# Optimization experiments

Measured on AMD Instinct MI355X. Metric: run time of the kernel, lower is better.

The kernel has to match this reference:

```python
import jax, jax.numpy as jnp
import numpy as np

N_CONTEXT = 256  # teacher-forced prefix length (n_context)
N_INPUTS = 2
HID = 16         # LSTM hidden_size
PROJ = 2         # LSTM proj_size


def setup_inputs() -> dict:
    key = jax.random.key(0)
    ks = jax.random.split(key, 6)
    B, T = 4096, 1024
    s = 1.0 / np.sqrt(HID)  # torch LSTM init range
    return {
        "u_train": jax.random.normal(ks[0], (B, T, N_INPUTS + PROJ), jnp.float32),
        "w_ih": jax.random.uniform(ks[1], (4 * HID, N_INPUTS), jnp.float32, -s, s),
        "w_hh": jax.random.uniform(ks[2], (4 * HID, PROJ), jnp.float32, -s, s),
        "b_ih": jax.random.uniform(ks[3], (4 * HID,), jnp.float32, -s, s),
        "b_hh": jax.random.uniform(ks[4], (4 * HID,), jnp.float32, -s, s),
        "w_hr": jax.random.uniform(ks[5], (PROJ, HID), jnp.float32, -s, s),
    }


def _cell(x, h, c, w_ih, w_hh, b, w_hr):
    # PyTorch LSTM gate order: i, f, g, o; projected output h = (o*tanh(c)) @ w_hr.T
    gates = x @ w_ih.T + h @ w_hh.T + b  # [B, 4*HID]
    i, f, g, o = jnp.split(gates, 4, axis=-1)
    c_new = jax.nn.sigmoid(f) * c + jax.nn.sigmoid(i) * jnp.tanh(g)
    h_new = (jax.nn.sigmoid(o) * jnp.tanh(c_new)) @ w_hr.T  # [B, PROJ]
    return h_new, c_new


def reference(u_train, w_ih, w_hh, b_ih, b_hh, w_hr):
    B = u_train.shape[0]
    u = u_train[..., :N_INPUTS]   # [B, T, 2] exogenous inputs
    y = u_train[..., N_INPUTS:]
    b = b_ih + b_hh

    xs_est = (jnp.swapaxes(u[:, :N_CONTEXT], 0, 1),  # [nstep, B, 2]
              jnp.swapaxes(y[:, :N_CONTEXT], 0, 1))
    c0 = jnp.zeros((B, HID), u_train.dtype)

    def est_step(c, xy):
        x_t, y_t = xy
        h_new, c_new = _cell(x_t, y_t, c, w_ih, w_hh, b, w_hr)
        return c_new, h_new

    cn, h_est = jax.lax.scan(est_step, c0, xs_est)  # h_est: [nstep, B, 2]
    hn = h_est[-1]

    # ---- predict_state: free-running LSTM from (hn, cn) ----
    def pred_step(carry, x_t):
        h, c = carry
        h_new, c_new = _cell(x_t, h, c, w_ih, w_hh, b, w_hr)
        return (h_new, c_new), h_new

    _, h_pred = jax.lax.scan(pred_step, (hn, cn), jnp.swapaxes(u[:, N_CONTEXT:], 0, 1))

    return jnp.concatenate([jnp.swapaxes(h_est, 0, 1), jnp.swapaxes(h_pred, 0, 1)], axis=1)
```

## Files before the change

kernel.cpp:

```cpp
#include <hip/hip_runtime.h>

#define N_CTX  256
#define T_LEN  1024
#define N_SEQ  4096
#define CHUNK  16

__device__ __forceinline__ float fexp2(float x){ return __builtin_amdgcn_exp2f(x); }
__device__ __forceinline__ float frcp (float x){ return __builtin_amdgcn_rcpf(x); }

__device__ __forceinline__ float sigm(float x){
    return frcp(1.0f + fexp2(-1.4426950408889634f * x));
}
__device__ __forceinline__ float tanh_fast(float x){
    float a = fexp2(fminf(2.8853901631790583f * x, 126.0f));
    return (a - 1.0f) * frcp(a + 1.0f);
}

template<int CTRL>
__device__ __forceinline__ float dpp_add(float x){
    int y = __builtin_amdgcn_mov_dpp(__float_as_int(x), CTRL, 0xf, 0xf, true);
    return x + __int_as_float(y);
}
__device__ __forceinline__ float red16(float x){
    x = dpp_add<0xB1>(x);
    x = dpp_add<0x4E>(x);
    x = dpp_add<0x124>(x);
    x = dpp_add<0x128>(x);
    return x;
}

struct LaneW {
    float wi0[4], wi1[4], wh0[4], wh1[4], bs[4];
    float whr0, whr1;
};

template<bool TEACHER>
__device__ __forceinline__ void lstm_step(const float4 x, const LaneW& L,
                                          float& c, float& rh0, float& rh1)
{
    const float h0 = TEACHER ? x.z : rh0;
    const float h1 = TEACHER ? x.w : rh1;
    float g[4];
#pragma unroll
    for (int q = 0; q < 4; ++q)
        g[q] = fmaf(h1, L.wh1[q], fmaf(h0, L.wh0[q],
               fmaf(x.y, L.wi1[q], fmaf(x.x, L.wi0[q], L.bs[q]))));
    const float si = sigm(g[0]);
    const float sf = sigm(g[1]);
    const float tg = tanh_fast(g[2]);
    const float so = sigm(g[3]);
    c = fmaf(sf, c, si * tg);
    const float s = so * tanh_fast(c);
    rh0 = red16(s * L.whr0);
    rh1 = red16(s * L.whr1);
}

__device__ __forceinline__ void load_chunk(float4* b, const float4* __restrict__ up, int base){
#pragma unroll
    for (int i = 0; i < CHUNK; ++i) b[i] = up[base + i];
}

template<bool TEACHER>
__device__ __forceinline__ void compute_chunk(const float4* b, int base, const LaneW& L,
                                              float& c, float& rh0, float& rh1,
                                              float2* __restrict__ op, int j)
{
#pragma unroll
    for (int i = 0; i < CHUNK; ++i) {
        lstm_step<TEACHER>(b[i], L, c, rh0, rh1);
        if (j == 0) op[base + i] = make_float2(rh0, rh1);
    }
}

__global__ __launch_bounds__(256) void openlstm_kernel(
    const float* __restrict__ u,
    const float* __restrict__ w_ih,
    const float* __restrict__ w_hh,
    const float* __restrict__ b_ih,
    const float* __restrict__ b_hh,
    const float* __restrict__ w_hr,
    float* __restrict__ out)
{
    const int tid = blockIdx.x * blockDim.x + threadIdx.x;
    const int seq = tid >> 4;
    const int j   = tid & 15;

    LaneW L;
#pragma unroll
    for (int q = 0; q < 4; ++q) {
        const int row = q * 16 + j;
        L.wi0[q] = w_ih[row*2+0];
        L.wi1[q] = w_ih[row*2+1];
        L.wh0[q] = w_hh[row*2+0];
        L.wh1[q] = w_hh[row*2+1];
        L.bs[q]  = b_ih[row] + b_hh[row];
    }
    L.whr0 = w_hr[j];
    L.whr1 = w_hr[16+j];

    const float4* __restrict__ up = (const float4*)u + (size_t)seq * T_LEN;
    float2* __restrict__ op = (float2*)out + (size_t)seq * T_LEN;

    float c = 0.0f, rh0 = 0.0f, rh1 = 0.0f;
    float4 bufA[CHUNK], bufB[CHUNK];

    load_chunk(bufA, up, 0);

#pragma unroll 1
    for (int base = 0; base < N_CTX; base += 2*CHUNK) {
        load_chunk(bufB, up, base + CHUNK);
        compute_chunk<true>(bufA, base, L, c, rh0, rh1, op, j);
        load_chunk(bufA, up, base + 2*CHUNK);
        compute_chunk<true>(bufB, base + CHUNK, L, c, rh0, rh1, op, j);
    }

#pragma unroll 1
    for (int base = N_CTX; base < T_LEN; base += 2*CHUNK) {
        load_chunk(bufB, up, base + CHUNK);
        compute_chunk<false>(bufA, base, L, c, rh0, rh1, op, j);
        if (base + 2*CHUNK < T_LEN)
            load_chunk(bufA, up, base + 2*CHUNK);
        compute_chunk<false>(bufB, base + CHUNK, L, c, rh0, rh1, op, j);
    }
}

extern "C" void kernel_launch(void* const* d_in, const int* in_sizes, int n_in,
                              void* d_out, int out_size, void* d_ws, size_t ws_size,
                              hipStream_t stream) {
    const float* u    = (const float*)d_in[0];
    const float* w_ih = (const float*)d_in[1];
    const float* w_hh = (const float*)d_in[2];
    const float* b_ih = (const float*)d_in[3];
    const float* b_hh = (const float*)d_in[4];
    const float* w_hr = (const float*)d_in[5];
    float* out = (float*)d_out;

    const int threads = 256;
    const int blocks  = (N_SEQ * 16) / threads;
    hipLaunchKernelGGL(openlstm_kernel, dim3(blocks), dim3(threads), 0, stream,
                       u, w_ih, w_hh, b_ih, b_hh, w_hr, out);
}
```

Baseline: 256.4 us.

## Precompute input gate terms per chunk, fuse sigmoid-tanh divisions, pack FMAs, vectorize stores

Moves the input-dependent gate contributions (x·W_ih + bias) off the serial recurrence by computing them for a whole chunk ahead of the chain, using packed 2-wide FMAs. Inside each step it merges sigmoid(i)*tanh(g) and sigmoid(o)*tanh(c) into single reciprocals, so each step issues fewer rcp instructions on the dependent path. Outputs are now buffered and written as float4 pairs every four steps instead of one float2 per step, the two loops are merged into one chunk loop with a prefetch distance of two chunks, and launch bounds request one block per CU. The per-chunk transformed arrays and deeper prefetch raise register pressure.

```diff
diff --git a/kernel.cpp b/kernel.cpp
--- a/kernel.cpp
+++ b/kernel.cpp
@@ -4,17 +4,18 @@
 #define T_LEN  1024
 #define N_SEQ  4096
 #define CHUNK  16
+#define NCHUNK (T_LEN / CHUNK)
+#define CTXCK  (N_CTX / CHUNK)
+
+typedef float v2f __attribute__((ext_vector_type(2)));
 
 __device__ __forceinline__ float fexp2(float x){ return __builtin_amdgcn_exp2f(x); }
 __device__ __forceinline__ float frcp (float x){ return __builtin_amdgcn_rcpf(x); }
+__device__ __forceinline__ v2f pk_fma(v2f a, v2f b, v2f c){ return __builtin_elementwise_fma(a, b, c); }
 
-__device__ __forceinline__ float sigm(float x){
-    return frcp(1.0f + fexp2(-1.4426950408889634f * x));
-}
-__device__ __forceinline__ float tanh_fast(float x){
-    float a = fexp2(fminf(2.8853901631790583f * x, 126.0f));
-    return (a - 1.0f) * frcp(a + 1.0f);
-}
+#define L1C 1.4426950408889634f
+#define L2C 2.8853901631790583f
+#define ECLAMP 60.0f
 
 template<int CTRL>
 __device__ __forceinline__ float dpp_add(float x){
@@ -30,49 +31,78 @@
 }
 
 struct LaneW {
-    float wi0[4], wi1[4], wh0[4], wh1[4], bs[4];
+    v2f wi0_if, wi1_if, wi0_go, wi1_go;
+    v2f wh0_if, wh1_if, wh0_go, wh1_go;
+    v2f bs_if, bs_go;
     float whr0, whr1;
 };
 
-template<bool TEACHER>
-__device__ __forceinline__ void lstm_step(const float4 x, const LaneW& L,
-                                          float& c, float& rh0, float& rh1)
-{
-    const float h0 = TEACHER ? x.z : rh0;
-    const float h1 = TEACHER ? x.w : rh1;
-    float g[4];
-#pragma unroll
-    for (int q = 0; q < 4; ++q)
-        g[q] = fmaf(h1, L.wh1[q], fmaf(h0, L.wh0[q],
-               fmaf(x.y, L.wi1[q], fmaf(x.x, L.wi0[q], L.bs[q]))));
-    const float si = sigm(g[0]);
-    const float sf = sigm(g[1]);
-    const float tg = tanh_fast(g[2]);
-    const float so = sigm(g[3]);
-    c = fmaf(sf, c, si * tg);
-    const float s = so * tanh_fast(c);
-    rh0 = red16(s * L.whr0);
-    rh1 = red16(s * L.whr1);
-}
+struct ChunkX {
+    v2f   xif[CHUNK];
+    v2f   xgo[CHUNK];
+    float y0[CHUNK];
+    float y1[CHUNK];
+};
 
 __device__ __forceinline__ void load_chunk(float4* b, const float4* __restrict__ up, int base){
 #pragma unroll
     for (int i = 0; i < CHUNK; ++i) b[i] = up[base + i];
 }
 
-template<bool TEACHER>
-__device__ __forceinline__ void compute_chunk(const float4* b, int base, const LaneW& L,
-                                              float& c, float& rh0, float& rh1,
-                                              float2* __restrict__ op, int j)
-{
+__device__ __forceinline__ void transform_chunk(ChunkX& X, const float4* raw, const LaneW& L){
 #pragma unroll
     for (int i = 0; i < CHUNK; ++i) {
-        lstm_step<TEACHER>(b[i], L, c, rh0, rh1);
-        if (j == 0) op[base + i] = make_float2(rh0, rh1);
+        const float4 x = raw[i];
+        v2f xx = {x.x, x.x}, xy = {x.y, x.y};
+        X.xif[i] = pk_fma(xy, L.wi1_if, pk_fma(xx, L.wi0_if, L.bs_if));
+        X.xgo[i] = pk_fma(xy, L.wi1_go, pk_fma(xx, L.wi0_go, L.bs_go));
+        X.y0[i]  = x.z;
+        X.y1[i]  = x.w;
     }
 }
 
-__global__ __launch_bounds__(256) void openlstm_kernel(
+template<bool TEACHER>
+__device__ __forceinline__ void lstm_step(v2f xif, v2f xgo, float y0, float y1,
+                                          const LaneW& L, float& c, float& rh0, float& rh1)
+{
+    const float h0 = TEACHER ? y0 : rh0;
+    const float h1 = TEACHER ? y1 : rh1;
+    v2f hh0 = {h0, h0}, hh1 = {h1, h1};
+    v2f gif = pk_fma(hh1, L.wh1_if, pk_fma(hh0, L.wh0_if, xif));
+    v2f ggo = pk_fma(hh1, L.wh1_go, pk_fma(hh0, L.wh0_go, xgo));
+    const float u  = fexp2(fminf(gif.x * -L1C, ECLAMP));
+    const float ef = fexp2(fminf(gif.y * -L1C, ECLAMP));
+    const float v  = fexp2(fminf(ggo.x *  L2C, ECLAMP));
+    const float eo = fexp2(fminf(ggo.y * -L1C, ECLAMP));
+    const float sf   = frcp(1.0f + ef);
+    const float sitg = (v - 1.0f) * frcp((1.0f + u) * (v + 1.0f));
+    c = fmaf(sf, c, sitg);
+    const float w = fexp2(fminf(c * L2C, ECLAMP));
+    const float s = (w - 1.0f) * frcp((1.0f + eo) * (w + 1.0f));
+    rh0 = red16(s * L.whr0);
+    rh1 = red16(s * L.whr1);
+}
+
+template<bool TEACHER>
+__device__ __forceinline__ void chain_chunk(const ChunkX& X, int baseT, const LaneW& L,
+                                            float& c, float& rh0, float& rh1,
+                                            float4* __restrict__ opv, bool store_lane)
+{
+    float o[8];
+#pragma unroll
+    for (int i = 0; i < CHUNK; ++i) {
+        lstm_step<TEACHER>(X.xif[i], X.xgo[i], X.y0[i], X.y1[i], L, c, rh0, rh1);
+        o[(i & 3) * 2]     = rh0;
+        o[(i & 3) * 2 + 1] = rh1;
+        if ((i & 3) == 3 && store_lane) {
+            const int f4i = (baseT + i - 3) >> 1;
+            opv[f4i]     = make_float4(o[0], o[1], o[2], o[3]);
+            opv[f4i + 1] = make_float4(o[4], o[5], o[6], o[7]);
+        }
+    }
+}
+
+__global__ __launch_bounds__(256, 1) void openlstm_kernel(
     const float* __restrict__ u,
     const float* __restrict__ w_ih,
     const float* __restrict__ w_hh,
@@ -86,41 +116,48 @@
     const int j   = tid & 15;
 
     LaneW L;
-#pragma unroll
-    for (int q = 0; q < 4; ++q) {
-        const int row = q * 16 + j;
-        L.wi0[q] = w_ih[row*2+0];
-        L.wi1[q] = w_ih[row*2+1];
-        L.wh0[q] = w_hh[row*2+0];
-        L.wh1[q] = w_hh[row*2+1];
-        L.bs[q]  = b_ih[row] + b_hh[row];
+    {
+        const int ri = j, rf = 16 + j, rg = 32 + j, ro = 48 + j;
+        L.wi0_if = (v2f){w_ih[ri*2+0], w_ih[rf*2+0]};
+        L.wi1_if = (v2f){w_ih[ri*2+1], w_ih[rf*2+1]};
+        L.wi0_go = (v2f){w_ih[rg*2+0], w_ih[ro*2+0]};
+        L.wi1_go = (v2f){w_ih[rg*2+1], w_ih[ro*2+1]};
+        L.wh0_if = (v2f){w_hh[ri*2+0], w_hh[rf*2+0]};
+        L.wh1_if = (v2f){w_hh[ri*2+1], w_hh[rf*2+1]};
+        L.wh0_go = (v2f){w_hh[rg*2+0], w_hh[ro*2+0]};
+        L.wh1_go = (v2f){w_hh[rg*2+1], w_hh[ro*2+1]};
+        L.bs_if  = (v2f){b_ih[ri] + b_hh[ri], b_ih[rf] + b_hh[rf]};
+        L.bs_go  = (v2f){b_ih[rg] + b_hh[rg], b_ih[ro] + b_hh[ro]};
+        L.whr0   = w_hr[j];
+        L.whr1   = w_hr[16 + j];
     }
-    L.whr0 = w_hr[j];
-    L.whr1 = w_hr[16+j];
 
     const float4* __restrict__ up = (const float4*)u + (size_t)seq * T_LEN;
-    float2* __restrict__ op = (float2*)out + (size_t)seq * T_LEN;
+    float4* __restrict__ opv = (float4*)((float2*)out + (size_t)seq * T_LEN);
+    const bool sl = (j == 0);
 
     float c = 0.0f, rh0 = 0.0f, rh1 = 0.0f;
-    float4 bufA[CHUNK], bufB[CHUNK];
+    float4 rawA[CHUNK], rawB[CHUNK];
 
-    load_chunk(bufA, up, 0);
+    load_chunk(rawA, up, 0);
+    load_chunk(rawB, up, CHUNK);
 
 #pragma unroll 1
-    for (int base = 0; base < N_CTX; base += 2*CHUNK) {
-        load_chunk(bufB, up, base + CHUNK);
-        compute_chunk<true>(bufA, base, L, c, rh0, rh1, op, j);
-        load_chunk(bufA, up, base + 2*CHUNK);
-        compute_chunk<true>(bufB, base + CHUNK, L, c, rh0, rh1, op, j);
-    }
-
-#pragma unroll 1
-    for (int base = N_CTX; base < T_LEN; base += 2*CHUNK) {
-        load_chunk(bufB, up, base + CHUNK);
-        compute_chunk<false>(bufA, base, L, c, rh0, rh1, op, j);
-        if (base + 2*CHUNK < T_LEN)
-            load_chunk(bufA, up, base + 2*CHUNK);
-        compute_chunk<false>(bufB, base + CHUNK, L, c, rh0, rh1, op, j);
+    for (int ck = 0; ck < NCHUNK; ck += 2) {
+        {
+            ChunkX XA;
+            transform_chunk(XA, rawA, L);
+            if (ck + 2 < NCHUNK) load_chunk(rawA, up, (ck + 2) * CHUNK);
+            if (ck < CTXCK) chain_chunk<true >(XA, ck * CHUNK, L, c, rh0, rh1, opv, sl);
+            else            chain_chunk<false>(XA, ck * CHUNK, L, c, rh0, rh1, opv, sl);
+        }
+        {
+            ChunkX XB;
+            transform_chunk(XB, rawB, L);
+            if (ck + 3 < NCHUNK) load_chunk(rawB, up, (ck + 3) * CHUNK);
+            if (ck + 1 < CTXCK) chain_chunk<true >(XB, (ck + 1) * CHUNK, L, c, rh0, rh1, opv, sl);
+            else                chain_chunk<false>(XB, (ck + 1) * CHUNK, L, c, rh0, rh1, opv, sl);
+        }
     }
 }
 
```

New measurement: 251.7 us. Within noise of the previous version (-1.8%).
